# Kernel optimization log

Hardware: AMD Instinct MI355X
Metric: run time of the kernel (lower is better)

Reference implementation:

```python
import jax, jax.numpy as jnp
import numpy as np

S, B, H, N = 512, 32, 512, 131072  # seq_len, batch, hidden_dim, num candidate spans
MAX_STEP = 20  # max_length


def setup_inputs() -> dict:
    key = jax.random.key(0)
    ks = jax.random.split(key, 8)
    hidden = jax.random.normal(ks[0], (S, B, 2 * H), dtype=jnp.float32)
    span_bids = jax.random.randint(ks[1], (N,), 0, B, dtype=jnp.int32)
    # begin in [1, S-1-MAX_STEP-1] so that begin-1>=0 and end=begin+step <= S-1
    span_begins = jax.random.randint(ks[2], (N,), 1, S - MAX_STEP - 2, dtype=jnp.int32)
    steps = jax.random.randint(ks[3], (N,), 2, MAX_STEP + 1, dtype=jnp.int32)
    span_ends = span_begins + steps
    span_flags = jax.random.randint(ks[4], (N,), 0, 2, dtype=jnp.int32)
    span_weights = jax.random.uniform(ks[5], (N,), dtype=jnp.float32)
    W1 = jax.random.normal(ks[6], (2 * H, H), dtype=jnp.float32) / np.sqrt(2.0 * H)
    b1 = jnp.zeros((H,), dtype=jnp.float32)
    W2 = jax.random.normal(ks[7], (H, 1), dtype=jnp.float32) / np.sqrt(float(H))
    b2 = jnp.zeros((1,), dtype=jnp.float32)
    return {"hidden": hidden, "span_bids": span_bids, "span_begins": span_begins,
            "span_ends": span_ends, "span_flags": span_flags, "span_weights": span_weights,
            "W1": W1, "b1": b1, "W2": W2, "b2": b2}


def reference(hidden, span_bids, span_begins, span_ends, span_flags, span_weights, W1, b1, W2, b2):
    h = W2.shape[0]  # hidden_dim
    # vectorized _span_embed: fwd diff on first half, bwd diff on second half
    fwd = hidden[span_ends - 1, span_bids, :h] - hidden[span_begins - 1, span_bids, :h]
    bwd = hidden[span_begins, span_bids, h:] - hidden[span_ends, span_bids, h:]
    feats = jnp.concatenate([fwd, bwd], axis=-1)  # [N, 2H]
    z = jnp.maximum(feats @ W1 + b1, 0.0)
    p = jax.nn.sigmoid(z @ W2 + b2)[:, 0]  # [N]
    targets = (span_flags == 1).astype(p.dtype)
    n_pos = jnp.sum(targets)
    n_tot = jnp.asarray(targets.shape[0], p.dtype)
    scale = 2.0 * n_pos / n_tot  # negative weights scaled by 2*P/(P+N)
    w_eff = jnp.where(span_flags == 1, span_weights, span_weights * scale)
    pc = jnp.clip(p, 1e-7, 1.0 - 1e-7)
    bce = -(targets * jnp.log(pc) + (1.0 - targets) * jnp.log(1.0 - pc))
    loss = jnp.mean(w_eff * bce)
    return loss
```

## Files before the change

kernel.cpp:

```cpp
#include <hip/hip_runtime.h>
#include <hip/hip_bf16.h>


typedef float f32x4 __attribute__((ext_vector_type(4)));
typedef float f32x2 __attribute__((ext_vector_type(2)));
typedef __bf16 bf16x8 __attribute__((ext_vector_type(8)));
typedef __bf16 bf16x4 __attribute__((ext_vector_type(4)));

__device__ __forceinline__ unsigned short f2bf(float f) {
  unsigned int u = __float_as_uint(f);
  u += 0x7fffu + ((u >> 16) & 1u);
  return (unsigned short)(u >> 16);
}
__device__ __forceinline__ float bf2f(unsigned int lo16) {
  return __uint_as_float(lo16 << 16);
}

__global__ void prep(const float* __restrict__ W1,
                     unsigned short* __restrict__ W1b,
                     const int* __restrict__ bids, int* __restrict__ ghist,
                     int nspans) {
  __shared__ int h[32];
  int t = threadIdx.x;
  if (blockIdx.x < 256) {
    int idx = blockIdx.x * 256 + t;
    int kc = idx & 3;
    int n  = (idx >> 2) & 511;
    int c  = idx >> 11;
    int k0 = c * 32 + kc * 8;
    unsigned short tmp[8];
#pragma unroll
    for (int j = 0; j < 8; ++j)
      tmp[j] = f2bf(W1[(k0 + j) * 512 + n]);
    *(uint4*)(W1b + c * 16384 + n * 32 + kc * 8) = *(uint4*)tmp;
  } else {
    if (t < 32) h[t] = 0;
    __syncthreads();
    int base = (blockIdx.x - 256) * 1024;
#pragma unroll
    for (int i = 0; i < 4; ++i) {
      int idx = base + t + i * 256;
      if (idx < nspans) atomicAdd(&h[bids[idx]], 1);
    }
    __syncthreads();
    if (t < 32) atomicAdd(&ghist[t], h[t]);
  }
}

__global__ void span_scatter(const int* __restrict__ bids,
                             const int* __restrict__ ghist,
                             int* __restrict__ gslot,
                             int* __restrict__ sidx, int nspans) {
  __shared__ int lh[32], lbase[32], lcur[32];
  int t = threadIdx.x;
  if (t < 32) lh[t] = 0;
  __syncthreads();
  int base = blockIdx.x * 512;
  int myb[2];
#pragma unroll
  for (int i = 0; i < 2; ++i) {
    int idx = base + t + i * 256;
    myb[i] = (idx < nspans) ? bids[idx] : -1;
    if (myb[i] >= 0) atomicAdd(&lh[myb[i]], 1);
  }
  __syncthreads();
  if (t < 32) {
    int pre = 0;
    for (int j = 0; j < t; ++j) pre += ghist[j];
    lbase[t] = pre + atomicAdd(&gslot[t], lh[t]);
    lcur[t] = 0;
  }
  __syncthreads();
#pragma unroll
  for (int i = 0; i < 2; ++i) {
    int b = myb[i];
    if (b >= 0) {
      int pos = lbase[b] + atomicAdd(&lcur[b], 1);
      sidx[pos] = base + t + i * 256;
    }
  }
}

#define APITCH 522
__global__ __launch_bounds__(512, 4) void proj_gemm(
    const float* __restrict__ hidden,
    const unsigned short* __restrict__ w1b,
    unsigned char* __restrict__ Wq) {
  __shared__ __align__(16) unsigned short AH[64 * APITCH];
  unsigned short* Eb = AH;

  const int t = threadIdx.x;
  const int lane = t & 63;
  const int w = t >> 6;
  const int r0 = blockIdx.x << 6;
  const int hk = blockIdx.y << 9;
  const int q = lane >> 4;
  const int m = lane & 15;

  {
    const float* gbase = hidden + hk + (lane << 2);
#pragma unroll
    for (int i = 0; i < 8; ++i) {
      int row = (w << 3) + i;
      const float* rp = gbase + ((r0 + row) << 10);
#pragma unroll
      for (int hh = 0; hh < 2; ++hh) {
        float4 f = *(const float4*)(rp + (hh << 8));
        bf16x4 hv;
        hv[0] = (__bf16)f.x; hv[1] = (__bf16)f.y;
        hv[2] = (__bf16)f.z; hv[3] = (__bf16)f.w;
        *(bf16x4*)(AH + row * APITCH + (hh << 8) + (lane << 2)) = hv;
      }
    }
  }
  __syncthreads();

  int boffn[4];
#pragma unroll
  for (int nt = 0; nt < 4; ++nt)
    boffn[nt] = (((w << 6) + (nt << 4) + m) << 5) + (q << 3);
  const unsigned short* w1base = w1b + (blockIdx.y << 18);

  f32x4 acc[4][4];
#pragma unroll
  for (int i = 0; i < 4; ++i)
#pragma unroll
    for (int j = 0; j < 4; ++j) acc[i][j] = (f32x4){0.f, 0.f, 0.f, 0.f};

#pragma unroll
  for (int it = 0; it < 16; ++it) {
    const unsigned short* bt = w1base + (it << 14);
    bf16x8 bfr[4];
#pragma unroll
    for (int nt = 0; nt < 4; ++nt)
      bfr[nt] = *(const bf16x8*)(bt + boffn[nt]);
    bf16x8 af[4];
#pragma unroll
    for (int mt = 0; mt < 4; ++mt)
      af[mt] = *(const bf16x8*)(AH + ((mt << 4) + m) * APITCH + (it << 5) + (q << 3));
#pragma unroll
    for (int mt = 0; mt < 4; ++mt)
#pragma unroll
      for (int nt = 0; nt < 4; ++nt)
        acc[mt][nt] = __builtin_amdgcn_mfma_f32_16x16x32_bf16(af[mt], bfr[nt],
                                                              acc[mt][nt], 0, 0, 0);
  }
  __syncthreads();

  unsigned short* Ew = Eb + w * (32 * 72);
#pragma unroll
  for (int pass = 0; pass < 2; ++pass) {
#pragma unroll
    for (int mh = 0; mh < 2; ++mh) {
      int mt = (pass << 1) + mh;
#pragma unroll
      for (int r = 0; r < 4; ++r) {
        int rr = (mh << 4) + ((lane >> 4) << 2) + r;
#pragma unroll
        for (int nt = 0; nt < 4; ++nt)
          Ew[rr * 72 + (nt << 4) + m] = f2bf(acc[mt][nt][r]);
      }
    }
#pragma unroll
    for (int i = 0; i < 4; ++i) {
      int task = (i << 6) + lane;
      int rr = task >> 3;
      int ck = task & 7;
      uint4 v = *(const uint4*)&Ew[rr * 72 + (ck << 3)];
      float f0 = bf2f(v.x & 0xffff), f1 = bf2f(v.x >> 16);
      float f2 = bf2f(v.y & 0xffff), f3 = bf2f(v.y >> 16);
      float f4 = bf2f(v.z & 0xffff), f5 = bf2f(v.z >> 16);
      float f6 = bf2f(v.w & 0xffff), f7 = bf2f(v.w >> 16);
      uint2 o;
      o.x = __builtin_amdgcn_cvt_pk_fp8_f32(f0, f1, 0, false);
      o.x = __builtin_amdgcn_cvt_pk_fp8_f32(f2, f3, o.x, true);
      o.y = __builtin_amdgcn_cvt_pk_fp8_f32(f4, f5, 0, false);
      o.y = __builtin_amdgcn_cvt_pk_fp8_f32(f6, f7, o.y, true);
      int grow = r0 + (pass << 5) + rr;
      int col = (w << 6) + (ck << 3);
      if (hk == 0) {
        *(uint2*)(Wq + (grow << 10) + col) = o;
      } else if (grow >= 32) {
        *(uint2*)(Wq + ((grow - 32) << 10) + 512 + col) = o;
      }
    }
  }
}

#define SPB 64
__global__ __launch_bounds__(256) void span_eval(
    const unsigned char* __restrict__ Wq,
    const int* __restrict__ sidx,
    const int* __restrict__ bids, const int* __restrict__ begins,
    const int* __restrict__ ends, const int* __restrict__ flags,
    const float* __restrict__ weights,
    const float* __restrict__ b1, const float* __restrict__ w2,
    const float* __restrict__ b2, float* __restrict__ partials) {
  __shared__ int oB[SPB], oE[SPB], sfl[SPB];
  __shared__ float swt[SPB];
  __shared__ float red[4][3];
  const int t = threadIdx.x;
  const int lane = t & 63;
  const int w = t >> 6;
  const int h = lane >> 5;
  const int hl = lane & 31;

  const int nblk = gridDim.x;
  int lb = blockIdx.x;
  if ((nblk & 7) == 0) {
    const int cpx = nblk >> 3;
    lb = (blockIdx.x & 7) * cpx + (blockIdx.x >> 3);
  }
  const int sbase = lb * SPB;

  if (t < SPB) {
    int s = sidx[sbase + t];
    int b = bids[s], bg = begins[s], en = ends[s];
    oB[t] = (((bg - 1) << 5) + b) << 10;
    oE[t] = (((en - 1) << 5) + b) << 10;
    sfl[t] = flags[s];
    swt[t] = weights[s];
  }
  __syncthreads();

  const int sp0 = ((w << 1) + h) << 3;
  const int c0 = hl << 4;
  float b1v[16], w2v[16];
#pragma unroll
  for (int qq = 0; qq < 4; ++qq) {
    float4 bv = *(const float4*)(b1 + c0 + (qq << 2));
    float4 wv = *(const float4*)(w2 + c0 + (qq << 2));
    b1v[(qq << 2) + 0] = bv.x; b1v[(qq << 2) + 1] = bv.y;
    b1v[(qq << 2) + 2] = bv.z; b1v[(qq << 2) + 3] = bv.w;
    w2v[(qq << 2) + 0] = wv.x; w2v[(qq << 2) + 1] = wv.y;
    w2v[(qq << 2) + 2] = wv.z; w2v[(qq << 2) + 3] = wv.w;
  }

  auto dec = [](unsigned int v, float* f) {
    f32x2 a = __builtin_amdgcn_cvt_pk_f32_fp8(v, false);
    f32x2 b = __builtin_amdgcn_cvt_pk_f32_fp8(v, true);
    f[0] = a[0]; f[1] = a[1]; f[2] = b[0]; f[3] = b[1];
  };

  uint4 BU[3], BV[3], EU[3], EV[3];
  auto ld = [&](int slot, int j) {
    int ob = oB[sp0 + j], oe = oE[sp0 + j];
    BU[slot] = *(const uint4*)(Wq + ob + c0);
    BV[slot] = *(const uint4*)(Wq + ob + 512 + c0);
    EU[slot] = *(const uint4*)(Wq + oe + c0);
    EV[slot] = *(const uint4*)(Wq + oe + 512 + c0);
  };
  ld(0, 0); ld(1, 1); ld(2, 2);

  float mylogit = 0.f;
#pragma unroll
  for (int j = 0; j < 8; ++j) {
    const int slot = j % 3;
    float buf[16], bvf[16], euf[16], evf[16];
    dec(BU[slot].x, buf); dec(BU[slot].y, buf + 4);
    dec(BU[slot].z, buf + 8); dec(BU[slot].w, buf + 12);
    dec(BV[slot].x, bvf); dec(BV[slot].y, bvf + 4);
    dec(BV[slot].z, bvf + 8); dec(BV[slot].w, bvf + 12);
    dec(EU[slot].x, euf); dec(EU[slot].y, euf + 4);
    dec(EU[slot].z, euf + 8); dec(EU[slot].w, euf + 12);
    dec(EV[slot].x, evf); dec(EV[slot].y, evf + 4);
    dec(EV[slot].z, evf + 8); dec(EV[slot].w, evf + 12);
    if (j + 3 < 8) ld(slot, j + 3);
    float sv = 0.f;
#pragma unroll
    for (int k = 0; k < 16; ++k) {
      float zp = euf[k] - buf[k] + bvf[k] - evf[k] + b1v[k];
      sv += fmaxf(zp, 0.f) * w2v[k];
    }
    sv += __shfl_xor(sv, 1);
    sv += __shfl_xor(sv, 2);
    sv += __shfl_xor(sv, 4);
    sv += __shfl_xor(sv, 8);
    sv += __shfl_xor(sv, 16);
    if (hl == j) mylogit = sv;
  }

  mylogit = __shfl(mylogit, ((lane & 8) << 2) + (lane & 7));

  float pos_t = 0.f, neg_t = 0.f, cnt_t = 0.f;
  if (lane < 16) {
    int sl = (w << 4) + lane;
    float logit = mylogit + b2[0];
    float p = 1.f / (1.f + expf(-logit));
    p = fminf(fmaxf(p, 1e-7f), 1.f - 1e-7f);
    int fl = sfl[sl];
    float bce = (fl == 1) ? -logf(p) : -logf(1.f - p);
    float term = swt[sl] * bce;
    pos_t = (fl == 1) ? term : 0.f;
    neg_t = (fl == 1) ? 0.f : term;
    cnt_t = (fl == 1) ? 1.f : 0.f;
  }
#pragma unroll
  for (int off = 1; off < 64; off <<= 1) {
    pos_t += __shfl_xor(pos_t, off);
    neg_t += __shfl_xor(neg_t, off);
    cnt_t += __shfl_xor(cnt_t, off);
  }
  if (lane == 0) { red[w][0] = pos_t; red[w][1] = neg_t; red[w][2] = cnt_t; }
  __syncthreads();
  if (t == 0) {
    partials[(blockIdx.x << 2) + 0] = red[0][0] + red[1][0] + red[2][0] + red[3][0];
    partials[(blockIdx.x << 2) + 1] = red[0][1] + red[1][1] + red[2][1] + red[3][1];
    partials[(blockIdx.x << 2) + 2] = red[0][2] + red[1][2] + red[2][2] + red[3][2];
  }
}

__global__ void finalize(const float* __restrict__ parts, int nblk,
                         float* __restrict__ out, int nspans) {
  __shared__ float sp[4], sn[4], sc[4];
  float P = 0.f, Ng = 0.f, C = 0.f;
  for (int i = threadIdx.x; i < nblk; i += 256) {
    P += parts[(i << 2) + 0];
    Ng += parts[(i << 2) + 1];
    C += parts[(i << 2) + 2];
  }
#pragma unroll
  for (int off = 1; off < 64; off <<= 1) {
    P += __shfl_xor(P, off);
    Ng += __shfl_xor(Ng, off);
    C += __shfl_xor(C, off);
  }
  int w = threadIdx.x >> 6;
  if ((threadIdx.x & 63) == 0) { sp[w] = P; sn[w] = Ng; sc[w] = C; }
  __syncthreads();
  if (threadIdx.x == 0) {
    P = sp[0] + sp[1] + sp[2] + sp[3];
    Ng = sn[0] + sn[1] + sn[2] + sn[3];
    C = sc[0] + sc[1] + sc[2] + sc[3];
    float scale = 2.f * C / (float)nspans;
    out[0] = (P + scale * Ng) / (float)nspans;
  }
}

extern "C" void kernel_launch(void* const* d_in, const int* in_sizes, int n_in,
                              void* d_out, int out_size, void* d_ws, size_t ws_size,
                              hipStream_t stream) {
  const float* hidden = (const float*)d_in[0];
  const int* bids     = (const int*)d_in[1];
  const int* begins   = (const int*)d_in[2];
  const int* ends     = (const int*)d_in[3];
  const int* flags    = (const int*)d_in[4];
  const float* weights = (const float*)d_in[5];
  const float* W1 = (const float*)d_in[6];
  const float* b1 = (const float*)d_in[7];
  const float* W2 = (const float*)d_in[8];
  const float* b2 = (const float*)d_in[9];
  float* out = (float*)d_out;
  const int nspans = in_sizes[1];
  const int nblk = nspans / SPB;

  float* partials = (float*)d_ws;
  unsigned short* W1b = (unsigned short*)((char*)d_ws + (1 << 18));
  unsigned char* Wq = (unsigned char*)((char*)d_ws + (2 << 20));
  int* ghist = (int*)((char*)d_ws + (19 << 20));
  int* gslot = ghist + 32;
  int* sidx  = (int*)((char*)d_ws + (20 << 20));

  hipMemsetAsync(ghist, 0, 64 * sizeof(int), stream);
  prep<<<384, 256, 0, stream>>>(W1, W1b, bids, ghist, nspans);
  span_scatter<<<(nspans + 511) / 512, 256, 0, stream>>>(bids, ghist, gslot,
                                                         sidx, nspans);
  proj_gemm<<<dim3(256, 2), 512, 0, stream>>>(hidden, W1b, Wq);
  span_eval<<<nblk, 256, 0, stream>>>(Wq, sidx, bids, begins, ends, flags,
                                      weights, b1, W2, b2, partials);
  finalize<<<1, 256, 0, stream>>>(partials, nblk, out, nspans);
}
```

Baseline: 173.4 us.

## Store A tile in MFMA fragment layout and write fp8 output directly from accumulators

The hidden tile is now staged in LDS already arranged in MFMA-fragment order, so A-operand reads are contiguous and need no padded pitch. The epilogue drops the LDS round-trip (bf16 staging, barrier, re-read) and packs accumulator values straight into fp8 words. Because this permutes the column order stored in Wq, span_eval now reads b1/w2 with a matching permuted index. In exchange, global stores become 4-byte scattered writes, and the global loads of hidden become less coalesced.

```diff
diff --git a/kernel.cpp b/kernel.cpp
--- a/kernel.cpp
+++ b/kernel.cpp
@@ -81,13 +81,11 @@
   }
 }
 
-#define APITCH 522
 __global__ __launch_bounds__(512, 4) void proj_gemm(
     const float* __restrict__ hidden,
     const unsigned short* __restrict__ w1b,
     unsigned char* __restrict__ Wq) {
-  __shared__ __align__(16) unsigned short AH[64 * APITCH];
-  unsigned short* Eb = AH;
+  __shared__ __align__(16) unsigned short LB[32768];
 
   const int t = threadIdx.x;
   const int lane = t & 63;
@@ -98,18 +96,27 @@
   const int m = lane & 15;
 
   {
-    const float* gbase = hidden + hk + (lane << 2);
-#pragma unroll
-    for (int i = 0; i < 8; ++i) {
-      int row = (w << 3) + i;
-      const float* rp = gbase + ((r0 + row) << 10);
-#pragma unroll
-      for (int hh = 0; hh < 2; ++hh) {
-        float4 f = *(const float4*)(rp + (hh << 8));
-        bf16x4 hv;
-        hv[0] = (__bf16)f.x; hv[1] = (__bf16)f.y;
-        hv[2] = (__bf16)f.z; hv[3] = (__bf16)f.w;
-        *(bf16x4*)(AH + row * APITCH + (hh << 8) + (lane << 2)) = hv;
+    const int kq = lane >> 4;
+    const int sm = lane & 15;
+#pragma unroll
+    for (int ii = 0; ii < 2; ++ii) {
+      const int it = (w << 1) + ii;
+#pragma unroll
+      for (int mt = 0; mt < 4; ++mt) {
+#pragma unroll
+        for (int hh = 0; hh < 2; ++hh) {
+          const int kk_ = (hh << 4) + (kq << 2);
+          const float* gp = hidden + ((r0 + (mt << 4) + sm) << 10)
+                                   + hk + (it << 5) + kk_;
+          float4 f = *(const float4*)gp;
+          bf16x4 hv;
+          hv[0] = (__bf16)f.x; hv[1] = (__bf16)f.y;
+          hv[2] = (__bf16)f.z; hv[3] = (__bf16)f.w;
+          const int qq = kk_ >> 3;
+          const int kkr = kk_ & 7;
+          *(bf16x4*)(LB + (((it << 2) + mt) << 9)
+                        + (((qq << 4) + sm) << 3) + kkr) = hv;
+        }
       }
     }
   }
@@ -137,7 +144,8 @@
     bf16x8 af[4];
 #pragma unroll
     for (int mt = 0; mt < 4; ++mt)
-      af[mt] = *(const bf16x8*)(AH + ((mt << 4) + m) * APITCH + (it << 5) + (q << 3));
+      af[mt] = *(const bf16x8*)(LB + (((it << 2) + mt) << 9)
+                                   + (((q << 4) + m) << 3));
 #pragma unroll
     for (int mt = 0; mt < 4; ++mt)
 #pragma unroll
@@ -145,43 +153,23 @@
         acc[mt][nt] = __builtin_amdgcn_mfma_f32_16x16x32_bf16(af[mt], bfr[nt],
                                                               acc[mt][nt], 0, 0, 0);
   }
-  __syncthreads();
-
-  unsigned short* Ew = Eb + w * (32 * 72);
-#pragma unroll
-  for (int pass = 0; pass < 2; ++pass) {
-#pragma unroll
-    for (int mh = 0; mh < 2; ++mh) {
-      int mt = (pass << 1) + mh;
+
+  {
+    const int cb = (w << 6) + (m << 2);
+#pragma unroll
+    for (int mt = 0; mt < 4; ++mt) {
 #pragma unroll
       for (int r = 0; r < 4; ++r) {
-        int rr = (mh << 4) + ((lane >> 4) << 2) + r;
-#pragma unroll
-        for (int nt = 0; nt < 4; ++nt)
-          Ew[rr * 72 + (nt << 4) + m] = f2bf(acc[mt][nt][r]);
-      }
-    }
-#pragma unroll
-    for (int i = 0; i < 4; ++i) {
-      int task = (i << 6) + lane;
-      int rr = task >> 3;
-      int ck = task & 7;
-      uint4 v = *(const uint4*)&Ew[rr * 72 + (ck << 3)];
-      float f0 = bf2f(v.x & 0xffff), f1 = bf2f(v.x >> 16);
-      float f2 = bf2f(v.y & 0xffff), f3 = bf2f(v.y >> 16);
-      float f4 = bf2f(v.z & 0xffff), f5 = bf2f(v.z >> 16);
-      float f6 = bf2f(v.w & 0xffff), f7 = bf2f(v.w >> 16);
-      uint2 o;
-      o.x = __builtin_amdgcn_cvt_pk_fp8_f32(f0, f1, 0, false);
-      o.x = __builtin_amdgcn_cvt_pk_fp8_f32(f2, f3, o.x, true);
-      o.y = __builtin_amdgcn_cvt_pk_fp8_f32(f4, f5, 0, false);
-      o.y = __builtin_amdgcn_cvt_pk_fp8_f32(f6, f7, o.y, true);
-      int grow = r0 + (pass << 5) + rr;
-      int col = (w << 6) + (ck << 3);
-      if (hk == 0) {
-        *(uint2*)(Wq + (grow << 10) + col) = o;
-      } else if (grow >= 32) {
-        *(uint2*)(Wq + ((grow - 32) << 10) + 512 + col) = o;
+        unsigned int o = __builtin_amdgcn_cvt_pk_fp8_f32(
+            acc[mt][0][r], acc[mt][1][r], 0, false);
+        o = __builtin_amdgcn_cvt_pk_fp8_f32(
+            acc[mt][2][r], acc[mt][3][r], o, true);
+        int grow = r0 + (mt << 4) + (q << 2) + r;
+        if (hk == 0) {
+          *(unsigned int*)(Wq + (grow << 10) + cb) = o;
+        } else if (grow >= 32) {
+          *(unsigned int*)(Wq + ((grow - 32) << 10) + 512 + cb) = o;
+        }
       }
     }
   }
@@ -227,13 +215,10 @@
   const int c0 = hl << 4;
   float b1v[16], w2v[16];
 #pragma unroll
-  for (int qq = 0; qq < 4; ++qq) {
-    float4 bv = *(const float4*)(b1 + c0 + (qq << 2));
-    float4 wv = *(const float4*)(w2 + c0 + (qq << 2));
-    b1v[(qq << 2) + 0] = bv.x; b1v[(qq << 2) + 1] = bv.y;
-    b1v[(qq << 2) + 2] = bv.z; b1v[(qq << 2) + 3] = bv.w;
-    w2v[(qq << 2) + 0] = wv.x; w2v[(qq << 2) + 1] = wv.y;
-    w2v[(qq << 2) + 2] = wv.z; w2v[(qq << 2) + 3] = wv.w;
+  for (int j = 0; j < 16; ++j) {
+    int colp = ((hl >> 2) << 6) + ((j & 3) << 4) + ((hl & 3) << 2) + (j >> 2);
+    b1v[j] = b1[colp];
+    w2v[j] = w2[colp];
   }
 
   auto dec = [](unsigned int v, float* f) {
```

Measured after the change: 166.2 us. 4.1% less time.
